# Optimization experiments

Hardware: AMD Instinct MI355X
Metric: run time of the kernel (lower is better)

The kernel has to match this reference:

```python
import jax, jax.numpy as jnp
import numpy as np

B_SZ, T, H, N, L = 4, 512, 256, 64, 4
EPS = 1e-5

def _hippo(n):
    i = np.arange(n)[:, None]; j = np.arange(n)[None, :]
    A = np.where(i >= j, ((-1.0) ** (i - j)) * np.sqrt((2 * i + 1.0) * (2 * j + 1.0)), 0.0)
    # scale to be contractive so the 512-step dense recurrence stays finite
    A = A / (1.1 * np.linalg.norm(A, 2))
    return A.astype(np.float32)

def _xavier(key, shape):
    fan_in, fan_out = shape[1], shape[0]
    a = float(np.sqrt(6.0 / (fan_in + fan_out)))
    return jax.random.uniform(key, shape, jnp.float32, -a, a)

def setup_inputs() -> dict:
    key = jax.random.key(0)
    ks = jax.random.split(key, 8)
    x = jax.random.normal(ks[0], (B_SZ, T, H), jnp.float32)
    A = jnp.broadcast_to(jnp.asarray(_hippo(N)), (L, N, N))
    Bm = jnp.stack([_xavier(jax.random.fold_in(ks[1], l), (N, H)) for l in range(L)])
    Cm = jnp.stack([_xavier(jax.random.fold_in(ks[2], l), (H, N)) for l in range(L)])
    Dm = jnp.stack([_xavier(jax.random.fold_in(ks[3], l), (H, H)) for l in range(L)])
    Win = _xavier(ks[4], (H, H)); bin_ = jnp.zeros((H,), jnp.float32)
    Wout = _xavier(ks[5], (H, H)); bout = jnp.zeros((H,), jnp.float32)
    return {"x": x, "Win": Win, "bin_": bin_, "Wout": Wout, "bout": bout,
            "A": A, "Bm": Bm, "Cm": Cm, "Dm": Dm}

def _ln(x):
    m = jnp.mean(x, -1, keepdims=True)
    v = jnp.mean((x - m) ** 2, -1, keepdims=True)
    return (x - m) / jnp.sqrt(v + EPS)

def _ssm_layer(h, A, B, C, D):
    # h: (B,T,H); dense state (B,N,H)
    Cbar = C.mean(0)            # mean over output rows (matches C_state.mean(dim=2))
    BT = B.T                    # (H,N)
    DT = D.T                    # (H,H)
    def step(state, u):        # state (B,N,H), u (B,H)
        y = jnp.einsum('bnh,n->bh', state, Cbar) + u @ DT   # output uses pre-update state
        new_state = jnp.einsum('nm,bmh->bnh', A, state) + (u @ BT)[:, :, None]
        return new_state, y
    state0 = jnp.zeros((h.shape[0], A.shape[0], h.shape[2]), h.dtype)
    _, ys = jax.lax.scan(step, state0, jnp.swapaxes(h, 0, 1))  # scan over T
    y = jnp.swapaxes(ys, 0, 1)
    y = jax.nn.gelu(y, approximate=False) + h   # GELU -> (dropout=0) -> residual
    return _ln(y)

def reference(x, Win, bin_, Wout, bout, A, Bm, Cm, Dm):
    h = x @ Win.T + bin_
    for l in range(L):
        h = _ssm_layer(h, A[l], Bm[l], Cm[l], Dm[l])
    h = _ln(h)
    return h @ Wout.T + bout
```

## Files before the change

kernel.cpp:

```cpp
#include <hip/hip_runtime.h>

#define TSEQ 512
#define HDIM 256
#define NDIM 64
#define LC   48
#define YSTR 260
#define NWB  128

typedef __attribute__((ext_vector_type(4))) float  f32x4;
typedef __attribute__((ext_vector_type(8))) short  s16x8;
typedef __attribute__((ext_vector_type(4))) unsigned short u16x4;
typedef unsigned long long u64;
typedef unsigned short us;

#define MFMA16 __builtin_amdgcn_mfma_f32_16x16x32_bf16

__device__ __forceinline__ float wave_red(float v) {
#pragma unroll
    for (int m = 1; m < 64; m <<= 1) v += __shfl_xor(v, m, 64);
    return v;
}
__device__ __forceinline__ float lane_bcast(float v, int l) {
    return __int_as_float(__builtin_amdgcn_readlane(__float_as_int(v), l));
}
__device__ __forceinline__ us f2bf(float f) {
    unsigned u = __float_as_uint(f);
    u += 0x7fffu + ((u >> 16) & 1u);
    return (us)(u >> 16);
}
__device__ __forceinline__ float bf2f(us h) {
    return __uint_as_float(((unsigned)h) << 16);
}
__device__ __forceinline__ int swz(int row, int chunk) {
    return row * 512 + (((chunk) ^ (row & 7)) << 4);
}

__device__ __forceinline__ void st_mall(float* p, float v) {
    __hip_atomic_store(p, v, __ATOMIC_RELAXED, __HIP_MEMORY_SCOPE_AGENT);
}
__device__ __forceinline__ u64 ld_mall8(const u64* p) {
    return __hip_atomic_load(p, __ATOMIC_RELAXED, __HIP_MEMORY_SCOPE_AGENT);
}
__device__ __forceinline__ void flag_set(unsigned* f) {
    __hip_atomic_store(f, 1u, __ATOMIC_RELAXED, __HIP_MEMORY_SCOPE_AGENT);
}
__device__ __forceinline__ void flag_wait(const unsigned* f) {
    while (__hip_atomic_load(f, __ATOMIC_RELAXED, __HIP_MEMORY_SCOPE_AGENT) == 0u)
        __builtin_amdgcn_s_sleep(1);
}

__global__ void __launch_bounds__(256) k_prep(
    const float* __restrict__ Win, const float* __restrict__ Wout,
    const float* __restrict__ Bm, const float* __restrict__ Dm,
    const float* __restrict__ Cm, const float* __restrict__ A,
    us* __restrict__ Win_bf, us* __restrict__ Wout_bf,
    us* __restrict__ Bm_bf, us* __restrict__ Dm_bf,
    float* __restrict__ cbar_g, float* __restrict__ wA8,
    unsigned* __restrict__ flags)
{
    __shared__ __align__(16) float Pa[4096];
    __shared__ __align__(16) float Pb[4096];
    const int gid = blockIdx.x, tid = threadIdx.x;

    if (gid < 128) {
        for (int q = gid * 256 + tid; q < 114688; q += 32768) {
            const float* s; us* d; int off;
            if (q < 16384)      { s = Win;  d = Win_bf;  off = q; }
            else if (q < 32768) { s = Wout; d = Wout_bf; off = q - 16384; }
            else if (q < 49152) { s = Bm;   d = Bm_bf;   off = q - 32768; }
            else                { s = Dm;   d = Dm_bf;   off = q - 49152; }
            f32x4 v = ((const f32x4*)s)[off];
            u16x4 p; p[0] = f2bf(v[0]); p[1] = f2bf(v[1]); p[2] = f2bf(v[2]); p[3] = f2bf(v[3]);
            ((u16x4*)d)[off] = p;
        }
        return;
    }
    if (gid == 128) {
        for (int i = tid; i < 4 + 4 * NWB; i += 256)
            __hip_atomic_store(&flags[i], 0u, __ATOMIC_RELAXED, __HIP_MEMORY_SCOPE_AGENT);
        const int l = tid >> 6, n = tid & 63;
        const float* cp = Cm + (size_t)l * HDIM * NDIM + n;
        float s0 = 0.f, s1 = 0.f, s2 = 0.f, s3 = 0.f;
        for (int h = 0; h < HDIM; h += 4) {
            s0 += cp[(h + 0) * NDIM]; s1 += cp[(h + 1) * NDIM];
            s2 += cp[(h + 2) * NDIM]; s3 += cp[(h + 3) * NDIM];
        }
        cbar_g[tid] = ((s0 + s1) + (s2 + s3)) * (1.0f / HDIM);
        return;
    }
    for (int q = tid; q < 1024; q += 256) ((f32x4*)Pa)[q] = ((const f32x4*)A)[q];
    __syncthreads();
    const int r0 = (tid >> 3) * 2, c0 = (tid & 7) * 8;
    const f32x4 z4 = {0.f, 0.f, 0.f, 0.f};
#pragma unroll 1
    for (int it = 0; it < 3; ++it) {
        const float* S = (it & 1) ? Pb : Pa;
        float*       D = (it & 1) ? Pa : Pb;
        f32x4 s00 = z4, s01 = z4, s10 = z4, s11 = z4;
        for (int k = 0; k < 64; ++k) {
            float a0 = S[r0 * 64 + k], a1 = S[(r0 + 1) * 64 + k];
            f32x4 b0 = *(const f32x4*)(S + k * 64 + c0);
            f32x4 b1 = *(const f32x4*)(S + k * 64 + c0 + 4);
            s00 += a0 * b0; s01 += a0 * b1; s10 += a1 * b0; s11 += a1 * b1;
        }
        *(f32x4*)(D + r0 * 64 + c0) = s00;       *(f32x4*)(D + r0 * 64 + c0 + 4) = s01;
        *(f32x4*)(D + (r0 + 1) * 64 + c0) = s10; *(f32x4*)(D + (r0 + 1) * 64 + c0 + 4) = s11;
        __syncthreads();
    }
    for (int q = tid; q < 1024; q += 256) ((f32x4*)wA8)[q] = ((const f32x4*)Pb)[q];
}

__global__ void __launch_bounds__(512, 2) k_fused(
    const float* __restrict__ x, const float* __restrict__ bin,
    const float* __restrict__ bout, const float* __restrict__ A,
    const float* __restrict__ wA8, const float* __restrict__ cbar_g,
    const us* __restrict__ Win_bf, const us* __restrict__ Wout_bf,
    const us* __restrict__ Bm_bf, const us* __restrict__ Dm_bf,
    float* __restrict__ wbuf, float* __restrict__ BiA, float* __restrict__ BiB,
    unsigned* __restrict__ flags, float* __restrict__ out)
{
    __shared__ __align__(16) char smem[53568];
    us*    xl   = (us*)smem;
    float* yl   = (float*)(smem + 8192);
    float* bwin = (float*)(smem + 24832);
    float* wlds = (float*)(smem + 41216);
    float* cfin = (float*)(smem + 53504);

    const int gid = blockIdx.x, tid = threadIdx.x;
    const int lane = tid & 63, wv = tid >> 6;
    const int m = lane & 15, cgq = lane >> 4;
    const f32x4 z4 = {0.f, 0.f, 0.f, 0.f};

    if (gid == NWB) {
        float* As  = (float*)smem;
        float* A8s = (float*)(smem + 16384);
        float* uls = (float*)(smem + 32768);
        for (int q = tid; q < 1024; q += 512) {
            ((f32x4*)As)[q]  = ((const f32x4*)A)[q];
            ((f32x4*)A8s)[q] = ((const f32x4*)wA8)[q];
        }
        __syncthreads();
        if (wv < 4) {
            const int l = wv;
            float u = cbar_g[l * 64 + lane];
            uls[(l * 8 + 0) * 64 + lane] = u;
#pragma unroll 1
            for (int s = 1; s < 8; ++s) {
                float p0 = 0.f, p1 = 0.f, p2 = 0.f, p3 = 0.f;
#pragma unroll
                for (int k = 0; k < 64; k += 4) {
                    p0 += As[(k + 0) * 64 + lane] * lane_bcast(u, k + 0);
                    p1 += As[(k + 1) * 64 + lane] * lane_bcast(u, k + 1);
                    p2 += As[(k + 2) * 64 + lane] * lane_bcast(u, k + 2);
                    p3 += As[(k + 3) * 64 + lane] * lane_bcast(u, k + 3);
                }
                u = (p0 + p1) + (p2 + p3);
                uls[(l * 8 + s) * 64 + lane] = u;
            }
        }
        __syncthreads();
        {
            const int p = wv;
            float u0 = uls[(0 * 8 + p) * 64 + lane];
            float u1 = uls[(1 * 8 + p) * 64 + lane];
            float u2 = uls[(2 * 8 + p) * 64 + lane];
            float u3 = uls[(3 * 8 + p) * 64 + lane];
#pragma unroll 1
            for (int k6 = 0; k6 < 6; ++k6) {
                const int j = p + 8 * k6;
                st_mall(&wbuf[(0 * LC + j) * 64 + lane], u0);
                st_mall(&wbuf[(1 * LC + j) * 64 + lane], u1);
                st_mall(&wbuf[(2 * LC + j) * 64 + lane], u2);
                st_mall(&wbuf[(3 * LC + j) * 64 + lane], u3);
                if (k6 < 5) {
                    float n0 = 0.f, n1 = 0.f, n2 = 0.f, n3 = 0.f;
#pragma unroll
                    for (int k = 0; k < 64; ++k) {
                        float a = A8s[k * 64 + lane];
                        n0 += a * lane_bcast(u0, k); n1 += a * lane_bcast(u1, k);
                        n2 += a * lane_bcast(u2, k); n3 += a * lane_bcast(u3, k);
                    }
                    u0 = n0; u1 = n1; u2 = n2; u3 = n3;
                }
            }
        }
        __syncthreads();
        if (tid < 4) flag_set(&flags[tid]);
        return;
    }

    const int b = gid >> 5, tb = gid & 31, t0 = tb * 16;
    const size_t grow = (size_t)(b * TSEQ + t0);

    {
        const f32x4* gs = (const f32x4*)(x + grow * HDIM);
#pragma unroll
        for (int k = 0; k < 2; ++k) {
            int q = tid + k * 512;
            int row = q >> 6, c4 = q & 63;
            f32x4 v = gs[q];
            u16x4 pk; pk[0] = f2bf(v[0]); pk[1] = f2bf(v[1]); pk[2] = f2bf(v[2]); pk[3] = f2bf(v[3]);
            *(u16x4*)((char*)xl + swz(row, c4 >> 1) + (c4 & 1) * 8) = pk;
        }
    }
    __syncthreads();

    {
        f32x4 accA = z4, accB = z4;
        const us* W0 = Win_bf + (size_t)(wv * 32 + m) * HDIM;
        const us* W1 = Win_bf + (size_t)(wv * 32 + 16 + m) * HDIM;
#pragma unroll
        for (int ks = 0; ks < 8; ++ks) {
            s16x8 av = *(const s16x8*)((const char*)xl + swz(m, ks * 4 + cgq));
            s16x8 b0 = *(const s16x8*)(W0 + ks * 32 + cgq * 8);
            s16x8 b1 = *(const s16x8*)(W1 + ks * 32 + cgq * 8);
            accA = MFMA16(av, b0, accA, 0, 0, 0);
            accB = MFMA16(av, b1, accB, 0, 0, 0);
        }
        __syncthreads();
        const int h0c = wv * 32 + m, h1c = wv * 32 + 16 + m;
        float bi0 = bin[h0c], bi1 = bin[h1c];
#pragma unroll
        for (int reg = 0; reg < 4; ++reg) {
            int trow = cgq * 4 + reg;
            *(us*)((char*)xl + swz(trow, h0c >> 3) + (h0c & 7) * 2) = f2bf(accA[reg] + bi0);
            *(us*)((char*)xl + swz(trow, h1c >> 3) + (h1c & 7) * 2) = f2bf(accB[reg] + bi1);
        }
    }
    __syncthreads();

    if (wv < 4) {
        f32x4 accb = z4;
        const us* B0 = Bm_bf + (size_t)(wv * 16 + m) * HDIM;
#pragma unroll
        for (int ks = 0; ks < 8; ++ks) {
            s16x8 av = *(const s16x8*)((const char*)xl + swz(m, ks * 4 + cgq));
            s16x8 bv = *(const s16x8*)(B0 + ks * 32 + cgq * 8);
            accb = MFMA16(av, bv, accb, 0, 0, 0);
        }
#pragma unroll
        for (int reg = 0; reg < 4; ++reg)
            st_mall(&BiA[(grow + cgq * 4 + reg) * NDIM + wv * 16 + m], accb[reg]);
    }
    __syncthreads();
    if (tid == 0) flag_set(&flags[4 + 0 * NWB + gid]);

#pragma unroll 1
    for (int l = 0; l < 4; ++l) {
        const us* Dl = Dm_bf + (size_t)l * HDIM * HDIM;
        const float* bi = (l & 1) ? BiB : BiA;
        float*       bo = (l & 1) ? BiA : BiB;

        f32x4 accA = z4, accB = z4;
        {
            const us* D0 = Dl + (size_t)(wv * 32 + m) * HDIM;
            const us* D1 = Dl + (size_t)(wv * 32 + 16 + m) * HDIM;
#pragma unroll
            for (int ks = 0; ks < 8; ++ks) {
                s16x8 av = *(const s16x8*)((const char*)xl + swz(m, ks * 4 + cgq));
                s16x8 b0 = *(const s16x8*)(D0 + ks * 32 + cgq * 8);
                s16x8 b1 = *(const s16x8*)(D1 + ks * 32 + cgq * 8);
                accA = MFMA16(av, b0, accA, 0, 0, 0);
                accB = MFMA16(av, b1, accB, 0, 0, 0);
            }
        }

        {
            const unsigned* fp = nullptr;
            if (lane == 3) fp = &flags[l];
            else if (lane < 3 && (tb - 1 - (int)lane) >= 0) fp = &flags[4 + l * NWB + gid - 1 - lane];
            if (fp) flag_wait(fp);
        }

        {
            const u64* ws8 = (const u64*)(wbuf + (size_t)l * LC * NDIM);
            for (int q = tid; q < LC * NDIM / 2; q += 512)
                ((u64*)wlds)[q] = ld_mall8(&ws8[q]);
            const u64* bi8 = (const u64*)(bi + (size_t)b * TSEQ * NDIM);
#pragma unroll
            for (int k = 0; k < 4; ++k) {
                int q = tid + k * 512;
                int r = q >> 5, cc = q & 31;
                int t = t0 - LC + r;
                ((u64*)bwin)[q] = (t >= 0) ? ld_mall8(&bi8[(size_t)t * 32 + cc]) : 0ull;
            }
        }
        __syncthreads();

        {
            const int r0 = wv * 2;
            float c0 = 0.f, c1 = 0.f;
            float v0 = bwin[(LC - 1 + r0) * NDIM + lane];
            float v1 = bwin[(LC + r0) * NDIM + lane];
#pragma unroll
            for (int j = 0; j < LC; ++j) {
                float wj = wlds[j * NDIM + lane];
                c0 += wj * v0; c1 += wj * v1;
                v1 = v0;
                int nr = LC - 2 + r0 - j; nr = nr < 0 ? 0 : nr;
                v0 = bwin[nr * NDIM + lane];
            }
            c0 = wave_red(c0); c1 = wave_red(c1);
            if (lane == 0) { cfin[r0] = c0; cfin[r0 + 1] = c1; }
        }
        __syncthreads();

#pragma unroll
        for (int nt = 0; nt < 2; ++nt) {
            int hcol = wv * 32 + nt * 16 + m;
#pragma unroll
            for (int reg = 0; reg < 4; ++reg) {
                int trow = cgq * 4 + reg;
                float val = (nt ? accB[reg] : accA[reg]) + cfin[trow];
                float g = 0.5f * val * (1.0f + erff(val * 0.70710678118654752f));
                float r = bf2f(*(const us*)((const char*)xl + swz(trow, hcol >> 3) + (hcol & 7) * 2));
                yl[trow * YSTR + hcol] = g + r;
            }
        }
        __syncthreads();

        {
            const bool last = (l == 3);
#pragma unroll
            for (int q = 0; q < 2; ++q) {
                int r = wv * 2 + q;
                f32x4 yv = *(const f32x4*)(yl + r * YSTR + lane * 4);
                float s = (yv[0] + yv[1]) + (yv[2] + yv[3]);
                float sq = yv[0] * yv[0] + yv[1] * yv[1] + yv[2] * yv[2] + yv[3] * yv[3];
                s = wave_red(s); sq = wave_red(sq);
                float mn = s * (1.0f / HDIM);
                float var = sq * (1.0f / HDIM) - mn * mn;
                float rs = rsqrtf(var + 1e-5f);
                if (last) { float vz = var * rs * rs; rs = rs * rsqrtf(vz + 1e-5f); }
                u16x4 zp;
                zp[0] = f2bf((yv[0] - mn) * rs); zp[1] = f2bf((yv[1] - mn) * rs);
                zp[2] = f2bf((yv[2] - mn) * rs); zp[3] = f2bf((yv[3] - mn) * rs);
                *(u16x4*)((char*)xl + swz(r, lane >> 1) + (lane & 1) * 8) = zp;
            }
        }
        __syncthreads();

        if (l < 3) {
            if (wv < 4) {
                f32x4 accb = z4;
                const us* B0 = Bm_bf + (size_t)(l + 1) * NDIM * HDIM + (size_t)(wv * 16 + m) * HDIM;
#pragma unroll
                for (int ks = 0; ks < 8; ++ks) {
                    s16x8 av = *(const s16x8*)((const char*)xl + swz(m, ks * 4 + cgq));
                    s16x8 bv = *(const s16x8*)(B0 + ks * 32 + cgq * 8);
                    accb = MFMA16(av, bv, accb, 0, 0, 0);
                }
#pragma unroll
                for (int reg = 0; reg < 4; ++reg)
                    st_mall(&bo[(grow + cgq * 4 + reg) * NDIM + wv * 16 + m], accb[reg]);
            }
            __syncthreads();
            if (tid == 0) flag_set(&flags[4 + (l + 1) * NWB + gid]);
        } else {
            f32x4 a2A = z4, a2B = z4;
            const us* W0 = Wout_bf + (size_t)(wv * 32 + m) * HDIM;
            const us* W1 = Wout_bf + (size_t)(wv * 32 + 16 + m) * HDIM;
#pragma unroll
            for (int ks = 0; ks < 8; ++ks) {
                s16x8 av = *(const s16x8*)((const char*)xl + swz(m, ks * 4 + cgq));
                s16x8 b0 = *(const s16x8*)(W0 + ks * 32 + cgq * 8);
                s16x8 b1 = *(const s16x8*)(W1 + ks * 32 + cgq * 8);
                a2A = MFMA16(av, b0, a2A, 0, 0, 0);
                a2B = MFMA16(av, b1, a2B, 0, 0, 0);
            }
#pragma unroll
            for (int nt = 0; nt < 2; ++nt) {
                int hcol = wv * 32 + nt * 16 + m;
                float bo2 = bout[hcol];
#pragma unroll
                for (int reg = 0; reg < 4; ++reg) {
                    int trow = cgq * 4 + reg;
                    out[(grow + trow) * HDIM + hcol] = (nt ? a2B[reg] : a2A[reg]) + bo2;
                }
            }
        }
    }
}

extern "C" void kernel_launch(void* const* d_in, const int* in_sizes, int n_in,
                              void* d_out, int out_size, void* d_ws, size_t ws_size,
                              hipStream_t stream) {
    (void)in_sizes; (void)n_in; (void)out_size; (void)ws_size;
    const float* x    = (const float*)d_in[0];
    const float* Win  = (const float*)d_in[1];
    const float* bin  = (const float*)d_in[2];
    const float* Wout = (const float*)d_in[3];
    const float* bout = (const float*)d_in[4];
    const float* A    = (const float*)d_in[5];
    const float* Bm   = (const float*)d_in[6];
    const float* Cm   = (const float*)d_in[7];
    const float* Dm   = (const float*)d_in[8];

    float* ws     = (float*)d_ws;
    float* wbuf   = ws;
    float* cbar_g = ws + 16384;
    float* wA8    = ws + 17408;
    float* biA    = ws + 21504;
    float* biB    = ws + 152576;
    unsigned* flags = (unsigned*)(ws + 283648);
    us* Win_bf  = (us*)(ws + 284672);
    us* Wout_bf = Win_bf + 65536;
    us* Bm_bf   = Wout_bf + 65536;
    us* Dm_bf   = Bm_bf + 65536;
    float* out  = (float*)d_out;

    k_prep<<<130, 256, 0, stream>>>(Win, Wout, Bm, Dm, Cm, A,
                                    Win_bf, Wout_bf, Bm_bf, Dm_bf, cbar_g, wA8, flags);
    k_fused<<<NWB + 1, 512, 0, stream>>>(x, bin, bout, A, wA8, cbar_g,
                                         Win_bf, Wout_bf, Bm_bf, Dm_bf,
                                         wbuf, biA, biB, flags, out);
}
```

Measured before the change: 71.94 us.

## Split kernel-weight producer, publish layer0 early, compute LN stats in registers

The producer block now uses all 8 waves to compute the A^s·cbar powers, using a precomputed A^4, and writes layer 0's conv weights first so its flag is raised before layers 1-3 are written. Worker blocks move the B projection and flag publish to the start of each layer, issued alongside the D matmul, and drop the fp32 y staging buffer. LayerNorm statistics are now reduced in registers with cross-wave partial sums held in shared memory. The aim is to shorten the producer's critical path and cut shared-memory round trips and barriers, at the cost of more shared memory and a dependence on the partial-stat reduction order.

Result: slower. 76.00 us (+5.7%).

```diff
diff --git a/kernel.cpp b/kernel.cpp
--- a/kernel.cpp
+++ b/kernel.cpp
@@ -4,7 +4,7 @@
 #define HDIM 256
 #define NDIM 64
 #define LC   48
-#define YSTR 260
+#define MT   16
 #define NWB  128
 
 typedef __attribute__((ext_vector_type(4))) float  f32x4;
@@ -15,11 +15,6 @@
 
 #define MFMA16 __builtin_amdgcn_mfma_f32_16x16x32_bf16
 
-__device__ __forceinline__ float wave_red(float v) {
-#pragma unroll
-    for (int m = 1; m < 64; m <<= 1) v += __shfl_xor(v, m, 64);
-    return v;
-}
 __device__ __forceinline__ float lane_bcast(float v, int l) {
     return __int_as_float(__builtin_amdgcn_readlane(__float_as_int(v), l));
 }
@@ -34,7 +29,6 @@
 __device__ __forceinline__ int swz(int row, int chunk) {
     return row * 512 + (((chunk) ^ (row & 7)) << 4);
 }
-
 __device__ __forceinline__ void st_mall(float* p, float v) {
     __hip_atomic_store(p, v, __ATOMIC_RELAXED, __HIP_MEMORY_SCOPE_AGENT);
 }
@@ -55,7 +49,7 @@
     const float* __restrict__ Cm, const float* __restrict__ A,
     us* __restrict__ Win_bf, us* __restrict__ Wout_bf,
     us* __restrict__ Bm_bf, us* __restrict__ Dm_bf,
-    float* __restrict__ cbar_g, float* __restrict__ wA8,
+    float* __restrict__ cbar_g, float* __restrict__ wA4, float* __restrict__ wA8,
     unsigned* __restrict__ flags)
 {
     __shared__ __align__(16) float Pa[4096];
@@ -107,24 +101,32 @@
         *(f32x4*)(D + (r0 + 1) * 64 + c0) = s10; *(f32x4*)(D + (r0 + 1) * 64 + c0 + 4) = s11;
         __syncthreads();
     }
-    for (int q = tid; q < 1024; q += 256) ((f32x4*)wA8)[q] = ((const f32x4*)Pb)[q];
+    for (int q = tid; q < 1024; q += 256) {
+        ((f32x4*)wA4)[q] = ((const f32x4*)Pa)[q];
+        ((f32x4*)wA8)[q] = ((const f32x4*)Pb)[q];
+    }
 }
 
 __global__ void __launch_bounds__(512, 2) k_fused(
     const float* __restrict__ x, const float* __restrict__ bin,
     const float* __restrict__ bout, const float* __restrict__ A,
-    const float* __restrict__ wA8, const float* __restrict__ cbar_g,
+    const float* __restrict__ wA4, const float* __restrict__ wA8,
+    const float* __restrict__ cbar_g,
     const us* __restrict__ Win_bf, const us* __restrict__ Wout_bf,
     const us* __restrict__ Bm_bf, const us* __restrict__ Dm_bf,
     float* __restrict__ wbuf, float* __restrict__ BiA, float* __restrict__ BiB,
     unsigned* __restrict__ flags, float* __restrict__ out)
 {
-    __shared__ __align__(16) char smem[53568];
+    __shared__ __align__(16) char smem[57344];
     us*    xl   = (us*)smem;
-    float* yl   = (float*)(smem + 8192);
-    float* bwin = (float*)(smem + 24832);
-    float* wlds = (float*)(smem + 41216);
-    float* cfin = (float*)(smem + 53504);
+    float* bwin = (float*)(smem + 8192);
+    float* wlds = (float*)(smem + 24576);
+    float* cfin = (float*)(smem + 36864);
+    float* pstat = (float*)(smem + 36928);
+    float* As  = (float*)smem;
+    float* A4s = (float*)(smem + 16384);
+    float* A8s = (float*)(smem + 32768);
+    float* uls = (float*)(smem + 49152);
 
     const int gid = blockIdx.x, tid = threadIdx.x;
     const int lane = tid & 63, wv = tid >> 6;
@@ -132,20 +134,29 @@
     const f32x4 z4 = {0.f, 0.f, 0.f, 0.f};
 
     if (gid == NWB) {
-        float* As  = (float*)smem;
-        float* A8s = (float*)(smem + 16384);
-        float* uls = (float*)(smem + 32768);
         for (int q = tid; q < 1024; q += 512) {
             ((f32x4*)As)[q]  = ((const f32x4*)A)[q];
+            ((f32x4*)A4s)[q] = ((const f32x4*)wA4)[q];
             ((f32x4*)A8s)[q] = ((const f32x4*)wA8)[q];
         }
         __syncthreads();
-        if (wv < 4) {
-            const int l = wv;
+        {
+            const int l = wv >> 1, hf = wv & 1;
             float u = cbar_g[l * 64 + lane];
-            uls[(l * 8 + 0) * 64 + lane] = u;
+            if (hf) {
+                float p0 = 0.f, p1 = 0.f, p2 = 0.f, p3 = 0.f;
+#pragma unroll
+                for (int k = 0; k < 64; k += 4) {
+                    p0 += A4s[(k + 0) * 64 + lane] * lane_bcast(u, k + 0);
+                    p1 += A4s[(k + 1) * 64 + lane] * lane_bcast(u, k + 1);
+                    p2 += A4s[(k + 2) * 64 + lane] * lane_bcast(u, k + 2);
+                    p3 += A4s[(k + 3) * 64 + lane] * lane_bcast(u, k + 3);
+                }
+                u = (p0 + p1) + (p2 + p3);
+            }
+            uls[(l * 8 + hf * 4 + 0) * 64 + lane] = u;
 #pragma unroll 1
-            for (int s = 1; s < 8; ++s) {
+            for (int s = 1; s < 4; ++s) {
                 float p0 = 0.f, p1 = 0.f, p2 = 0.f, p3 = 0.f;
 #pragma unroll
                 for (int k = 0; k < 64; k += 4) {
@@ -155,41 +166,54 @@
                     p3 += As[(k + 3) * 64 + lane] * lane_bcast(u, k + 3);
                 }
                 u = (p0 + p1) + (p2 + p3);
-                uls[(l * 8 + s) * 64 + lane] = u;
-            }
-        }
-        __syncthreads();
-        {
-            const int p = wv;
-            float u0 = uls[(0 * 8 + p) * 64 + lane];
-            float u1 = uls[(1 * 8 + p) * 64 + lane];
-            float u2 = uls[(2 * 8 + p) * 64 + lane];
-            float u3 = uls[(3 * 8 + p) * 64 + lane];
+                uls[(l * 8 + hf * 4 + s) * 64 + lane] = u;
+            }
+        }
+        __syncthreads();
+        {
+            float u = uls[wv * 64 + lane];
 #pragma unroll 1
             for (int k6 = 0; k6 < 6; ++k6) {
-                const int j = p + 8 * k6;
-                st_mall(&wbuf[(0 * LC + j) * 64 + lane], u0);
-                st_mall(&wbuf[(1 * LC + j) * 64 + lane], u1);
-                st_mall(&wbuf[(2 * LC + j) * 64 + lane], u2);
-                st_mall(&wbuf[(3 * LC + j) * 64 + lane], u3);
+                st_mall(&wbuf[(size_t)(wv + 8 * k6) * 64 + lane], u);
                 if (k6 < 5) {
-                    float n0 = 0.f, n1 = 0.f, n2 = 0.f, n3 = 0.f;
+                    float n0 = 0.f;
+#pragma unroll
+                    for (int k = 0; k < 64; ++k)
+                        n0 += A8s[k * 64 + lane] * lane_bcast(u, k);
+                    u = n0;
+                }
+            }
+        }
+        __syncthreads();
+        if (tid == 0) flag_set(&flags[0]);
+        {
+            float u1 = uls[(8 + wv) * 64 + lane];
+            float u2 = uls[(16 + wv) * 64 + lane];
+            float u3 = uls[(24 + wv) * 64 + lane];
+#pragma unroll 1
+            for (int k6 = 0; k6 < 6; ++k6) {
+                const int j = wv + 8 * k6;
+                st_mall(&wbuf[(size_t)(1 * LC + j) * 64 + lane], u1);
+                st_mall(&wbuf[(size_t)(2 * LC + j) * 64 + lane], u2);
+                st_mall(&wbuf[(size_t)(3 * LC + j) * 64 + lane], u3);
+                if (k6 < 5) {
+                    float n1 = 0.f, n2 = 0.f, n3 = 0.f;
 #pragma unroll
                     for (int k = 0; k < 64; ++k) {
                         float a = A8s[k * 64 + lane];
-                        n0 += a * lane_bcast(u0, k); n1 += a * lane_bcast(u1, k);
-                        n2 += a * lane_bcast(u2, k); n3 += a * lane_bcast(u3, k);
+                        n1 += a * lane_bcast(u1, k); n2 += a * lane_bcast(u2, k);
+                        n3 += a * lane_bcast(u3, k);
                     }
-                    u0 = n0; u1 = n1; u2 = n2; u3 = n3;
-                }
-            }
-        }
-        __syncthreads();
-        if (tid < 4) flag_set(&flags[tid]);
+                    u1 = n1; u2 = n2; u3 = n3;
+                }
+            }
+        }
+        __syncthreads();
+        if (tid < 3) flag_set(&flags[1 + tid]);
         return;
     }
 
-    const int b = gid >> 5, tb = gid & 31, t0 = tb * 16;
+    const int b = gid >> 5, tb = gid & 31, t0 = tb * MT;
     const size_t grow = (size_t)(b * TSEQ + t0);
 
     {
@@ -205,10 +229,11 @@
     }
     __syncthreads();
 
+    f32x4 hacc0, hacc1;
     {
         f32x4 accA = z4, accB = z4;
         const us* W0 = Win_bf + (size_t)(wv * 32 + m) * HDIM;
-        const us* W1 = Win_bf + (size_t)(wv * 32 + 16 + m) * HDIM;
+        const us* W1 = W0 + (size_t)16 * HDIM;
 #pragma unroll
         for (int ks = 0; ks < 8; ++ks) {
             s16x8 av = *(const s16x8*)((const char*)xl + swz(m, ks * 4 + cgq));
@@ -217,53 +242,54 @@
             accA = MFMA16(av, b0, accA, 0, 0, 0);
             accB = MFMA16(av, b1, accB, 0, 0, 0);
         }
-        __syncthreads();
-        const int h0c = wv * 32 + m, h1c = wv * 32 + 16 + m;
+        hacc0 = accA; hacc1 = accB;
+    }
+    __syncthreads();
+    {
+        const int h0c = wv * 32 + m, h1c = h0c + 16;
         float bi0 = bin[h0c], bi1 = bin[h1c];
 #pragma unroll
         for (int reg = 0; reg < 4; ++reg) {
             int trow = cgq * 4 + reg;
-            *(us*)((char*)xl + swz(trow, h0c >> 3) + (h0c & 7) * 2) = f2bf(accA[reg] + bi0);
-            *(us*)((char*)xl + swz(trow, h1c >> 3) + (h1c & 7) * 2) = f2bf(accB[reg] + bi1);
+            *(us*)((char*)xl + swz(trow, h0c >> 3) + (h0c & 7) * 2) = f2bf(hacc0[reg] + bi0);
+            *(us*)((char*)xl + swz(trow, h1c >> 3) + (h1c & 7) * 2) = f2bf(hacc1[reg] + bi1);
         }
     }
     __syncthreads();
-
-    if (wv < 4) {
-        f32x4 accb = z4;
-        const us* B0 = Bm_bf + (size_t)(wv * 16 + m) * HDIM;
-#pragma unroll
-        for (int ks = 0; ks < 8; ++ks) {
-            s16x8 av = *(const s16x8*)((const char*)xl + swz(m, ks * 4 + cgq));
-            s16x8 bv = *(const s16x8*)(B0 + ks * 32 + cgq * 8);
-            accb = MFMA16(av, bv, accb, 0, 0, 0);
-        }
-#pragma unroll
-        for (int reg = 0; reg < 4; ++reg)
-            st_mall(&BiA[(grow + cgq * 4 + reg) * NDIM + wv * 16 + m], accb[reg]);
-    }
-    __syncthreads();
-    if (tid == 0) flag_set(&flags[4 + 0 * NWB + gid]);
 
 #pragma unroll 1
     for (int l = 0; l < 4; ++l) {
+        float* bufl = (l & 1) ? BiB : BiA;
         const us* Dl = Dm_bf + (size_t)l * HDIM * HDIM;
-        const float* bi = (l & 1) ? BiB : BiA;
-        float*       bo = (l & 1) ? BiA : BiB;
-
-        f32x4 accA = z4, accB = z4;
+
+        if (wv < 4) {
+            f32x4 accb = z4;
+            const us* B0 = Bm_bf + (size_t)l * NDIM * HDIM + (size_t)(wv * 16 + m) * HDIM;
+#pragma unroll
+            for (int ks = 0; ks < 8; ++ks) {
+                s16x8 av = *(const s16x8*)((const char*)xl + swz(m, ks * 4 + cgq));
+                s16x8 bv = *(const s16x8*)(B0 + ks * 32 + cgq * 8);
+                accb = MFMA16(av, bv, accb, 0, 0, 0);
+            }
+#pragma unroll
+            for (int reg = 0; reg < 4; ++reg)
+                st_mall(&bufl[(grow + cgq * 4 + reg) * NDIM + wv * 16 + m], accb[reg]);
+        }
+        f32x4 dA0 = z4, dA1 = z4;
         {
             const us* D0 = Dl + (size_t)(wv * 32 + m) * HDIM;
-            const us* D1 = Dl + (size_t)(wv * 32 + 16 + m) * HDIM;
+            const us* D1 = D0 + (size_t)16 * HDIM;
 #pragma unroll
             for (int ks = 0; ks < 8; ++ks) {
                 s16x8 av = *(const s16x8*)((const char*)xl + swz(m, ks * 4 + cgq));
                 s16x8 b0 = *(const s16x8*)(D0 + ks * 32 + cgq * 8);
                 s16x8 b1 = *(const s16x8*)(D1 + ks * 32 + cgq * 8);
-                accA = MFMA16(av, b0, accA, 0, 0, 0);
-                accB = MFMA16(av, b1, accB, 0, 0, 0);
-            }
-        }
+                dA0 = MFMA16(av, b0, dA0, 0, 0, 0);
+                dA1 = MFMA16(av, b1, dA1, 0, 0, 0);
+            }
+        }
+        __syncthreads();
+        if (tid == 0) flag_set(&flags[4 + l * NWB + gid]);
 
         {
             const unsigned* fp = nullptr;
@@ -276,7 +302,7 @@
             const u64* ws8 = (const u64*)(wbuf + (size_t)l * LC * NDIM);
             for (int q = tid; q < LC * NDIM / 2; q += 512)
                 ((u64*)wlds)[q] = ld_mall8(&ws8[q]);
-            const u64* bi8 = (const u64*)(bi + (size_t)b * TSEQ * NDIM);
+            const u64* bi8 = (const u64*)(bufl + (size_t)b * TSEQ * NDIM);
 #pragma unroll
             for (int k = 0; k < 4; ++k) {
                 int q = tid + k * 512;
@@ -300,84 +326,86 @@
                 int nr = LC - 2 + r0 - j; nr = nr < 0 ? 0 : nr;
                 v0 = bwin[nr * NDIM + lane];
             }
-            c0 = wave_red(c0); c1 = wave_red(c1);
+#pragma unroll
+            for (int k = 1; k < 64; k <<= 1) {
+                c0 += __shfl_xor(c0, k, 64); c1 += __shfl_xor(c1, k, 64);
+            }
             if (lane == 0) { cfin[r0] = c0; cfin[r0 + 1] = c1; }
         }
         __syncthreads();
 
-#pragma unroll
-        for (int nt = 0; nt < 2; ++nt) {
-            int hcol = wv * 32 + nt * 16 + m;
+        f32x4 o0, o1;
+        {
+            const int c0i = wv * 32 + m, c1i = c0i + 16;
 #pragma unroll
             for (int reg = 0; reg < 4; ++reg) {
                 int trow = cgq * 4 + reg;
-                float val = (nt ? accB[reg] : accA[reg]) + cfin[trow];
-                float g = 0.5f * val * (1.0f + erff(val * 0.70710678118654752f));
-                float r = bf2f(*(const us*)((const char*)xl + swz(trow, hcol >> 3) + (hcol & 7) * 2));
-                yl[trow * YSTR + hcol] = g + r;
+                float cf = cfin[trow];
+                float v, g;
+                v = dA0[reg] + cf; g = 0.5f * v * (1.0f + erff(v * 0.70710678118654752f));
+                o0[reg] = g + bf2f(*(const us*)((const char*)xl + swz(trow, c0i >> 3) + (c0i & 7) * 2));
+                v = dA1[reg] + cf; g = 0.5f * v * (1.0f + erff(v * 0.70710678118654752f));
+                o1[reg] = g + bf2f(*(const us*)((const char*)xl + swz(trow, c1i >> 3) + (c1i & 7) * 2));
+            }
+#pragma unroll
+            for (int reg = 0; reg < 4; ++reg) {
+                float s = o0[reg] + o1[reg];
+                float q = o0[reg] * o0[reg] + o1[reg] * o1[reg];
+#pragma unroll
+                for (int k = 1; k < 16; k <<= 1) {
+                    s += __shfl_xor(s, k, 64); q += __shfl_xor(q, k, 64);
+                }
+                if (m == 0) {
+                    int row = cgq * 4 + reg;
+                    int idx = (wv * 16 + row) * 2;
+                    pstat[idx] = s; pstat[idx + 1] = q;
+                }
             }
         }
         __syncthreads();
 
         {
             const bool last = (l == 3);
-#pragma unroll
-            for (int q = 0; q < 2; ++q) {
-                int r = wv * 2 + q;
-                f32x4 yv = *(const f32x4*)(yl + r * YSTR + lane * 4);
-                float s = (yv[0] + yv[1]) + (yv[2] + yv[3]);
-                float sq = yv[0] * yv[0] + yv[1] * yv[1] + yv[2] * yv[2] + yv[3] * yv[3];
-                s = wave_red(s); sq = wave_red(sq);
+            const int c0i = wv * 32 + m, c1i = c0i + 16;
+#pragma unroll
+            for (int reg = 0; reg < 4; ++reg) {
+                int row = cgq * 4 + reg;
+                float s = 0.f, q = 0.f;
+#pragma unroll
+                for (int w = 0; w < 8; ++w) {
+                    s += pstat[(w * 16 + row) * 2];
+                    q += pstat[(w * 16 + row) * 2 + 1];
+                }
                 float mn = s * (1.0f / HDIM);
-                float var = sq * (1.0f / HDIM) - mn * mn;
+                float var = q * (1.0f / HDIM) - mn * mn;
                 float rs = rsqrtf(var + 1e-5f);
-                if (last) { float vz = var * rs * rs; rs = rs * rsqrtf(vz + 1e-5f); }
-                u16x4 zp;
-                zp[0] = f2bf((yv[0] - mn) * rs); zp[1] = f2bf((yv[1] - mn) * rs);
-                zp[2] = f2bf((yv[2] - mn) * rs); zp[3] = f2bf((yv[3] - mn) * rs);
-                *(u16x4*)((char*)xl + swz(r, lane >> 1) + (lane & 1) * 8) = zp;
-            }
-        }
-        __syncthreads();
-
-        if (l < 3) {
-            if (wv < 4) {
-                f32x4 accb = z4;
-                const us* B0 = Bm_bf + (size_t)(l + 1) * NDIM * HDIM + (size_t)(wv * 16 + m) * HDIM;
-#pragma unroll
-                for (int ks = 0; ks < 8; ++ks) {
-                    s16x8 av = *(const s16x8*)((const char*)xl + swz(m, ks * 4 + cgq));
-                    s16x8 bv = *(const s16x8*)(B0 + ks * 32 + cgq * 8);
-                    accb = MFMA16(av, bv, accb, 0, 0, 0);
-                }
-#pragma unroll
-                for (int reg = 0; reg < 4; ++reg)
-                    st_mall(&bo[(grow + cgq * 4 + reg) * NDIM + wv * 16 + m], accb[reg]);
-            }
-            __syncthreads();
-            if (tid == 0) flag_set(&flags[4 + (l + 1) * NWB + gid]);
-        } else {
-            f32x4 a2A = z4, a2B = z4;
-            const us* W0 = Wout_bf + (size_t)(wv * 32 + m) * HDIM;
-            const us* W1 = Wout_bf + (size_t)(wv * 32 + 16 + m) * HDIM;
-#pragma unroll
-            for (int ks = 0; ks < 8; ++ks) {
-                s16x8 av = *(const s16x8*)((const char*)xl + swz(m, ks * 4 + cgq));
-                s16x8 b0 = *(const s16x8*)(W0 + ks * 32 + cgq * 8);
-                s16x8 b1 = *(const s16x8*)(W1 + ks * 32 + cgq * 8);
-                a2A = MFMA16(av, b0, a2A, 0, 0, 0);
-                a2B = MFMA16(av, b1, a2B, 0, 0, 0);
-            }
-#pragma unroll
-            for (int nt = 0; nt < 2; ++nt) {
-                int hcol = wv * 32 + nt * 16 + m;
-                float bo2 = bout[hcol];
-#pragma unroll
-                for (int reg = 0; reg < 4; ++reg) {
-                    int trow = cgq * 4 + reg;
-                    out[(grow + trow) * HDIM + hcol] = (nt ? a2B[reg] : a2A[reg]) + bo2;
-                }
-            }
+                if (last) { float vz = var * rs * rs; rs *= rsqrtf(vz + 1e-5f); }
+                *(us*)((char*)xl + swz(row, c0i >> 3) + (c0i & 7) * 2) = f2bf((o0[reg] - mn) * rs);
+                *(us*)((char*)xl + swz(row, c1i >> 3) + (c1i & 7) * 2) = f2bf((o1[reg] - mn) * rs);
+            }
+        }
+        __syncthreads();
+    }
+
+    {
+        f32x4 a2A = z4, a2B = z4;
+        const us* W0 = Wout_bf + (size_t)(wv * 32 + m) * HDIM;
+        const us* W1 = W0 + (size_t)16 * HDIM;
+#pragma unroll
+        for (int ks = 0; ks < 8; ++ks) {
+            s16x8 av = *(const s16x8*)((const char*)xl + swz(m, ks * 4 + cgq));
+            s16x8 b0 = *(const s16x8*)(W0 + ks * 32 + cgq * 8);
+            s16x8 b1 = *(const s16x8*)(W1 + ks * 32 + cgq * 8);
+            a2A = MFMA16(av, b0, a2A, 0, 0, 0);
+            a2B = MFMA16(av, b1, a2B, 0, 0, 0);
+        }
+        const int h0c = wv * 32 + m, h1c = h0c + 16;
+        float bo0 = bout[h0c], bo1 = bout[h1c];
+#pragma unroll
+        for (int reg = 0; reg < 4; ++reg) {
+            int trow = cgq * 4 + reg;
+            out[(grow + trow) * HDIM + h0c] = a2A[reg] + bo0;
+            out[(grow + trow) * HDIM + h1c] = a2B[reg] + bo1;
         }
     }
 }
@@ -400,18 +428,19 @@
     float* wbuf   = ws;
     float* cbar_g = ws + 16384;
     float* wA8    = ws + 17408;
-    float* biA    = ws + 21504;
-    float* biB    = ws + 152576;
-    unsigned* flags = (unsigned*)(ws + 283648);
-    us* Win_bf  = (us*)(ws + 284672);
+    float* wA4    = ws + 21504;
+    float* biA    = ws + 25600;
+    float* biB    = ws + 156672;
+    unsigned* flags = (unsigned*)(ws + 287744);
+    us* Win_bf  = (us*)(ws + 288768);
     us* Wout_bf = Win_bf + 65536;
     us* Bm_bf   = Wout_bf + 65536;
     us* Dm_bf   = Bm_bf + 65536;
     float* out  = (float*)d_out;
 
     k_prep<<<130, 256, 0, stream>>>(Win, Wout, Bm, Dm, Cm, A,
-                                    Win_bf, Wout_bf, Bm_bf, Dm_bf, cbar_g, wA8, flags);
-    k_fused<<<NWB + 1, 512, 0, stream>>>(x, bin, bout, A, wA8, cbar_g,
+                                    Win_bf, Wout_bf, Bm_bf, Dm_bf, cbar_g, wA4, wA8, flags);
+    k_fused<<<NWB + 1, 512, 0, stream>>>(x, bin, bout, A, wA4, wA8, cbar_g,
                                          Win_bf, Wout_bf, Bm_bf, Dm_bf,
                                          wbuf, biA, biB, flags, out);
 }
```

## Publish layer-0 recurrence weights early and centralize neighbor flag waits

Applied to the files above, without the earlier changes.

The prep block now computes and stores layer 0's chunked A-power weights first and sets its flag before computing layers 1-3. This lets the main blocks start layer 0 sooner instead of waiting for all four layers. The per-lane flag polling (lanes 0-3 of every wave) is replaced by a single thread waiting on all flags, followed by a block barrier, and the spin-loop sleep is lengthened. The longer sleep and the serialized waits may add latency when flags arrive.

After: 67.46 us. -6.2%, faster.

```diff
diff --git a/kernel.cpp b/kernel.cpp
--- a/kernel.cpp
+++ b/kernel.cpp
@@ -4,7 +4,7 @@
 #define HDIM 256
 #define NDIM 64
 #define LC   48
-#define YSTR 260
+#define MT   16
 #define NWB  128
 
 typedef __attribute__((ext_vector_type(4))) float  f32x4;
@@ -15,11 +15,6 @@
 
 #define MFMA16 __builtin_amdgcn_mfma_f32_16x16x32_bf16
 
-__device__ __forceinline__ float wave_red(float v) {
-#pragma unroll
-    for (int m = 1; m < 64; m <<= 1) v += __shfl_xor(v, m, 64);
-    return v;
-}
 __device__ __forceinline__ float lane_bcast(float v, int l) {
     return __int_as_float(__builtin_amdgcn_readlane(__float_as_int(v), l));
 }
@@ -34,7 +29,6 @@
 __device__ __forceinline__ int swz(int row, int chunk) {
     return row * 512 + (((chunk) ^ (row & 7)) << 4);
 }
-
 __device__ __forceinline__ void st_mall(float* p, float v) {
     __hip_atomic_store(p, v, __ATOMIC_RELAXED, __HIP_MEMORY_SCOPE_AGENT);
 }
@@ -46,7 +40,7 @@
 }
 __device__ __forceinline__ void flag_wait(const unsigned* f) {
     while (__hip_atomic_load(f, __ATOMIC_RELAXED, __HIP_MEMORY_SCOPE_AGENT) == 0u)
-        __builtin_amdgcn_s_sleep(1);
+        __builtin_amdgcn_s_sleep(4);
 }
 
 __global__ void __launch_bounds__(256) k_prep(
@@ -161,35 +155,50 @@
         __syncthreads();
         {
             const int p = wv;
-            float u0 = uls[(0 * 8 + p) * 64 + lane];
-            float u1 = uls[(1 * 8 + p) * 64 + lane];
-            float u2 = uls[(2 * 8 + p) * 64 + lane];
-            float u3 = uls[(3 * 8 + p) * 64 + lane];
+            float u = uls[p * 64 + lane];
+#pragma unroll 1
+            for (int k6 = 0; k6 < 6; ++k6) {
+                st_mall(&wbuf[(size_t)(p + 8 * k6) * 64 + lane], u);
+                if (k6 < 5) {
+                    float n0 = 0.f;
+#pragma unroll
+                    for (int k = 0; k < 64; ++k)
+                        n0 += A8s[k * 64 + lane] * lane_bcast(u, k);
+                    u = n0;
+                }
+            }
+        }
+        __syncthreads();
+        if (tid == 0) flag_set(&flags[0]);
+        {
+            const int p = wv;
+            float u1 = uls[(8 + p) * 64 + lane];
+            float u2 = uls[(16 + p) * 64 + lane];
+            float u3 = uls[(24 + p) * 64 + lane];
 #pragma unroll 1
             for (int k6 = 0; k6 < 6; ++k6) {
                 const int j = p + 8 * k6;
-                st_mall(&wbuf[(0 * LC + j) * 64 + lane], u0);
-                st_mall(&wbuf[(1 * LC + j) * 64 + lane], u1);
-                st_mall(&wbuf[(2 * LC + j) * 64 + lane], u2);
-                st_mall(&wbuf[(3 * LC + j) * 64 + lane], u3);
+                st_mall(&wbuf[(size_t)(1 * LC + j) * 64 + lane], u1);
+                st_mall(&wbuf[(size_t)(2 * LC + j) * 64 + lane], u2);
+                st_mall(&wbuf[(size_t)(3 * LC + j) * 64 + lane], u3);
                 if (k6 < 5) {
-                    float n0 = 0.f, n1 = 0.f, n2 = 0.f, n3 = 0.f;
+                    float n1 = 0.f, n2 = 0.f, n3 = 0.f;
 #pragma unroll
                     for (int k = 0; k < 64; ++k) {
                         float a = A8s[k * 64 + lane];
-                        n0 += a * lane_bcast(u0, k); n1 += a * lane_bcast(u1, k);
-                        n2 += a * lane_bcast(u2, k); n3 += a * lane_bcast(u3, k);
+                        n1 += a * lane_bcast(u1, k); n2 += a * lane_bcast(u2, k);
+                        n3 += a * lane_bcast(u3, k);
                     }
-                    u0 = n0; u1 = n1; u2 = n2; u3 = n3;
-                }
-            }
-        }
-        __syncthreads();
-        if (tid < 4) flag_set(&flags[tid]);
+                    u1 = n1; u2 = n2; u3 = n3;
+                }
+            }
+        }
+        __syncthreads();
+        if (tid < 3) flag_set(&flags[1 + tid]);
         return;
     }
 
-    const int b = gid >> 5, tb = gid & 31, t0 = tb * 16;
+    const int b = gid >> 5, tb = gid & 31, t0 = tb * MT;
     const size_t grow = (size_t)(b * TSEQ + t0);
 
     {
@@ -208,7 +217,7 @@
     {
         f32x4 accA = z4, accB = z4;
         const us* W0 = Win_bf + (size_t)(wv * 32 + m) * HDIM;
-        const us* W1 = Win_bf + (size_t)(wv * 32 + 16 + m) * HDIM;
+        const us* W1 = W0 + (size_t)16 * HDIM;
 #pragma unroll
         for (int ks = 0; ks < 8; ++ks) {
             s16x8 av = *(const s16x8*)((const char*)xl + swz(m, ks * 4 + cgq));
@@ -218,7 +227,7 @@
             accB = MFMA16(av, b1, accB, 0, 0, 0);
         }
         __syncthreads();
-        const int h0c = wv * 32 + m, h1c = wv * 32 + 16 + m;
+        const int h0c = wv * 32 + m, h1c = h0c + 16;
         float bi0 = bin[h0c], bi1 = bin[h1c];
 #pragma unroll
         for (int reg = 0; reg < 4; ++reg) {
@@ -254,7 +263,7 @@
         f32x4 accA = z4, accB = z4;
         {
             const us* D0 = Dl + (size_t)(wv * 32 + m) * HDIM;
-            const us* D1 = Dl + (size_t)(wv * 32 + 16 + m) * HDIM;
+            const us* D1 = D0 + (size_t)16 * HDIM;
 #pragma unroll
             for (int ks = 0; ks < 8; ++ks) {
                 s16x8 av = *(const s16x8*)((const char*)xl + swz(m, ks * 4 + cgq));
@@ -265,12 +274,13 @@
             }
         }
 
-        {
-            const unsigned* fp = nullptr;
-            if (lane == 3) fp = &flags[l];
-            else if (lane < 3 && (tb - 1 - (int)lane) >= 0) fp = &flags[4 + l * NWB + gid - 1 - lane];
-            if (fp) flag_wait(fp);
-        }
+        if (tid == 0) {
+            flag_wait(&flags[l]);
+#pragma unroll
+            for (int nb = 1; nb <= 3; ++nb)
+                if (tb - nb >= 0) flag_wait(&flags[4 + l * NWB + gid - nb]);
+        }
+        __syncthreads();
 
         {
             const u64* ws8 = (const u64*)(wbuf + (size_t)l * LC * NDIM);
@@ -300,7 +310,10 @@
                 int nr = LC - 2 + r0 - j; nr = nr < 0 ? 0 : nr;
                 v0 = bwin[nr * NDIM + lane];
             }
-            c0 = wave_red(c0); c1 = wave_red(c1);
+#pragma unroll
+            for (int k = 1; k < 64; k <<= 1) {
+                c0 += __shfl_xor(c0, k, 64); c1 += __shfl_xor(c1, k, 64);
+            }
             if (lane == 0) { cfin[r0] = c0; cfin[r0 + 1] = c1; }
         }
         __syncthreads();
@@ -314,7 +327,7 @@
                 float val = (nt ? accB[reg] : accA[reg]) + cfin[trow];
                 float g = 0.5f * val * (1.0f + erff(val * 0.70710678118654752f));
                 float r = bf2f(*(const us*)((const char*)xl + swz(trow, hcol >> 3) + (hcol & 7) * 2));
-                yl[trow * YSTR + hcol] = g + r;
+                yl[trow * 260 + hcol] = g + r;
             }
         }
         __syncthreads();
@@ -324,10 +337,13 @@
 #pragma unroll
             for (int q = 0; q < 2; ++q) {
                 int r = wv * 2 + q;
-                f32x4 yv = *(const f32x4*)(yl + r * YSTR + lane * 4);
+                f32x4 yv = *(const f32x4*)(yl + r * 260 + lane * 4);
                 float s = (yv[0] + yv[1]) + (yv[2] + yv[3]);
                 float sq = yv[0] * yv[0] + yv[1] * yv[1] + yv[2] * yv[2] + yv[3] * yv[3];
-                s = wave_red(s); sq = wave_red(sq);
+#pragma unroll
+                for (int k = 1; k < 64; k <<= 1) {
+                    s += __shfl_xor(s, k, 64); sq += __shfl_xor(sq, k, 64);
+                }
                 float mn = s * (1.0f / HDIM);
                 float var = sq * (1.0f / HDIM) - mn * mn;
                 float rs = rsqrtf(var + 1e-5f);
@@ -359,7 +375,7 @@
         } else {
             f32x4 a2A = z4, a2B = z4;
             const us* W0 = Wout_bf + (size_t)(wv * 32 + m) * HDIM;
-            const us* W1 = Wout_bf + (size_t)(wv * 32 + 16 + m) * HDIM;
+            const us* W1 = W0 + (size_t)16 * HDIM;
 #pragma unroll
             for (int ks = 0; ks < 8; ++ks) {
                 s16x8 av = *(const s16x8*)((const char*)xl + swz(m, ks * 4 + cgq));
```
